# Optimization experiments

Hardware: AMD Instinct MI355X
Metric: run time of the kernel (lower is better)

The kernel has to match this reference:

```python
import jax, jax.numpy as jnp
import numpy as np

BETA = 0.25  # commitment_beta


def _mlp(x, Ws, bs):
    # hidden layers with ReLU, final linear layer without activation
    h = x
    for W, b in zip(Ws[:-1], bs[:-1]):
        h = jax.nn.relu(h @ W + b)
    return h @ Ws[-1] + bs[-1]


def _vq(r, cb):
    # r: [B, D], cb: [K, D]
    # squared L2 distances via expansion: ||r||^2 - 2 r.cb^T + ||cb||^2
    d = (jnp.sum(r * r, axis=1, keepdims=True)
         - 2.0 * (r @ cb.T)
         + jnp.sum(cb * cb, axis=1))  # [B, K]
    idx = jnp.argmin(d, axis=1)  # [B]
    e = cb[idx]  # [B, D]
    sg = jax.lax.stop_gradient
    # per-sample codebook + commitment loss
    loss = (jnp.mean((sg(r) - e) ** 2, axis=1)
            + BETA * jnp.mean((r - sg(e)) ** 2, axis=1))  # [B]
    # straight-through estimator
    z_q = r + sg(e - r)
    return z_q, loss, idx


def setup_inputs() -> dict:
    key = jax.random.key(0)
    ks = jax.random.split(key, 16)
    B, D_IN, H1, H2, D_LAT, K = 16384, 2048, 1024, 512, 256, 1024

    def lin(k, fan_in, fan_out):
        s = 1.0 / np.sqrt(fan_in)
        return jax.random.uniform(k, (fan_in, fan_out), jnp.float32, -s, s)

    return {
        "x": jax.random.normal(ks[0], (B, D_IN), jnp.float32),
        "enc_W1": lin(ks[1], D_IN, H1), "enc_b1": jnp.zeros((H1,), jnp.float32),
        "enc_W2": lin(ks[2], H1, H2), "enc_b2": jnp.zeros((H2,), jnp.float32),
        "enc_W3": lin(ks[3], H2, D_LAT), "enc_b3": jnp.zeros((D_LAT,), jnp.float32),
        "ln_g": jnp.ones((D_LAT,), jnp.float32),
        "ln_b": jnp.zeros((D_LAT,), jnp.float32),
        "cb0": jax.random.normal(ks[4], (K, D_LAT), jnp.float32) * 0.02,
        "cb1": jax.random.normal(ks[5], (K, D_LAT), jnp.float32) * 0.02,
        "cb2": jax.random.normal(ks[6], (K, D_LAT), jnp.float32) * 0.02,
        "dec_W1": lin(ks[7], D_LAT, H2), "dec_b1": jnp.zeros((H2,), jnp.float32),
        "dec_W2": lin(ks[8], H2, H1), "dec_b2": jnp.zeros((H1,), jnp.float32),
        "dec_W3": lin(ks[9], H1, D_IN), "dec_b3": jnp.zeros((D_IN,), jnp.float32),
    }


def reference(x, enc_W1, enc_b1, enc_W2, enc_b2, enc_W3, enc_b3,
              ln_g, ln_b, cb0, cb1, cb2,
              dec_W1, dec_b1, dec_W2, dec_b2, dec_W3, dec_b3):
    z = _mlp(x, [enc_W1, enc_W2, enc_W3], [enc_b1, enc_b2, enc_b3])
    # LayerNorm over latent dim
    mu = jnp.mean(z, axis=-1, keepdims=True)
    var = jnp.var(z, axis=-1, keepdims=True)
    z = (z - mu) * jax.lax.rsqrt(var + 1e-5) * ln_g + ln_b

    sg = jax.lax.stop_gradient
    residual = z
    z_q_total = jnp.zeros_like(z)
    losses, indices = [], []
    for cb in (cb0, cb1, cb2):
        z_q, vloss, idx = _vq(residual, cb)
        residual = residual - sg(z_q)
        z_q_total = z_q_total + z_q
        losses.append(vloss)
        indices.append(idx)

    x_hat = _mlp(z_q_total, [dec_W1, dec_W2, dec_W3], [dec_b1, dec_b2, dec_b3])
    recon_loss = jnp.mean((x_hat - x) ** 2, axis=1)  # [B]
    loss = jnp.sum(jnp.stack(losses, axis=1), axis=1) + recon_loss  # [B]
    idx_out = jnp.stack(indices, axis=1)  # [B, 3]
    return x_hat, loss, idx_out
```

## Files before the change

kernel.cpp:

```cpp
#include <hip/hip_runtime.h>
#include <stdint.h>

typedef __bf16 bf16x8 __attribute__((ext_vector_type(8)));
typedef _Float16 f16x8 __attribute__((ext_vector_type(8)));
typedef float f32x4 __attribute__((ext_vector_type(4)));

#define BETA 0.25f

__device__ __forceinline__ unsigned short f2bf(float f) {
    __bf16 h = (__bf16)f;
    return __builtin_bit_cast(unsigned short, h);
}

__device__ __forceinline__ unsigned short f2h(float f) {
    _Float16 h = (_Float16)f;
    return __builtin_bit_cast(unsigned short, h);
}

__device__ __forceinline__ void split8(const float* a, uint4& vh, uint4& vl) {
    unsigned h[8], l[8];
#pragma unroll
    for (int j = 0; j < 8; ++j) {
        _Float16 hi = (_Float16)a[j];
        float hf = (float)hi;
        _Float16 lo = (_Float16)((a[j] - hf) * 2048.0f);
        h[j] = (unsigned)__builtin_bit_cast(unsigned short, hi);
        l[j] = (unsigned)__builtin_bit_cast(unsigned short, lo);
    }
    vh.x = h[0] | (h[1] << 16); vh.y = h[2] | (h[3] << 16);
    vh.z = h[4] | (h[5] << 16); vh.w = h[6] | (h[7] << 16);
    vl.x = l[0] | (l[1] << 16); vl.y = l[2] | (l[3] << 16);
    vl.z = l[4] | (l[5] << 16); vl.w = l[6] | (l[7] << 16);
}

__global__ __launch_bounds__(256) void wsplit_t(
    const float* __restrict__ W, unsigned short* __restrict__ WTh,
    unsigned short* __restrict__ WTl, int K, int N)
{
    __shared__ float tile[32][33];
    const int t = threadIdx.x;
    const int n0 = blockIdx.x * 32, k0 = blockIdx.y * 32;
    const int rr = t >> 3, c4 = (t & 7) * 4;
    float4 w = *(const float4*)(W + (size_t)(k0 + rr) * N + n0 + c4);
    tile[rr][c4 + 0] = w.x; tile[rr][c4 + 1] = w.y;
    tile[rr][c4 + 2] = w.z; tile[rr][c4 + 3] = w.w;
    __syncthreads();
    float v[4] = {tile[c4 + 0][rr], tile[c4 + 1][rr],
                  tile[c4 + 2][rr], tile[c4 + 3][rr]};
    unsigned short hh[4], ll[4];
#pragma unroll
    for (int j = 0; j < 4; ++j) {
        float s = v[j] * 32.0f;
        _Float16 hi = (_Float16)s;
        float hf = (float)hi;
        hh[j] = __builtin_bit_cast(unsigned short, hi);
        ll[j] = f2h((s - hf) * 2048.0f);
    }
    ushort4 oh, ol;
    oh.x = hh[0]; oh.y = hh[1]; oh.z = hh[2]; oh.w = hh[3];
    ol.x = ll[0]; ol.y = ll[1]; ol.z = ll[2]; ol.w = ll[3];
    *(ushort4*)(WTh + (size_t)(n0 + rr) * K + k0 + c4) = oh;
    *(ushort4*)(WTl + (size_t)(n0 + rr) * K + k0 + c4) = ol;
}

template <bool AF32, bool RELU, bool OUTSPLIT>
__global__ __launch_bounds__(256, 2) void gemm_f16x2(
    const float* __restrict__ Af,
    const unsigned short* __restrict__ Ah, const unsigned short* __restrict__ Al,
    const unsigned short* __restrict__ WTh, const unsigned short* __restrict__ WTl,
    const float* __restrict__ bias,
    void* __restrict__ Oh, unsigned short* __restrict__ Ol,
    int M, int N, int K)
{
    __shared__ unsigned short Ash[2][128][36];
    __shared__ unsigned short Asl[2][128][36];
    __shared__ unsigned short Bsh[2][128][36];
    __shared__ unsigned short Bsl[2][128][36];

    const int t = threadIdx.x;
    const int m0 = blockIdx.y * 128, n0 = blockIdx.x * 128;
    const int wave = t >> 6, lane = t & 63;
    const int wm = wave & 1, wn = wave >> 1;
    const int l15 = lane & 15, kq = lane >> 4;

    f32x4 ach[4][4] = {};
    f32x4 acl[4][4] = {};

    const int sr = t >> 1, skc = (t & 1) * 16;

    float af[16];
    uint4 vah, vah2, val, val2;
    uint4 vbh, vbh2, vbl, vbl2;

    auto LOAD = [&](int kb) {
        if (AF32) {
            const float* ap = Af + (size_t)(m0 + sr) * K + kb + skc;
            *(float4*)&af[0]  = *(const float4*)(ap);
            *(float4*)&af[4]  = *(const float4*)(ap + 4);
            *(float4*)&af[8]  = *(const float4*)(ap + 8);
            *(float4*)&af[12] = *(const float4*)(ap + 12);
        } else {
            const unsigned short* aph = Ah + (size_t)(m0 + sr) * K + kb + skc;
            const unsigned short* apl = Al + (size_t)(m0 + sr) * K + kb + skc;
            vah  = *(const uint4*)(aph);
            vah2 = *(const uint4*)(aph + 8);
            val  = *(const uint4*)(apl);
            val2 = *(const uint4*)(apl + 8);
        }
        const unsigned short* bph = WTh + (size_t)(n0 + sr) * K + kb + skc;
        const unsigned short* bpl = WTl + (size_t)(n0 + sr) * K + kb + skc;
        vbh  = *(const uint4*)(bph);
        vbh2 = *(const uint4*)(bph + 8);
        vbl  = *(const uint4*)(bpl);
        vbl2 = *(const uint4*)(bpl + 8);
    };

    auto STORE = [&](int buf) {
        uint4 wah, wah2, wal, wal2;
        if (AF32) {
            split8(&af[0], wah, wal);
            split8(&af[8], wah2, wal2);
        } else {
            wah = vah; wah2 = vah2; wal = val; wal2 = val2;
        }
        *(uint4*)&Ash[buf][sr][skc]     = wah;
        *(uint4*)&Ash[buf][sr][skc + 8] = wah2;
        *(uint4*)&Asl[buf][sr][skc]     = wal;
        *(uint4*)&Asl[buf][sr][skc + 8] = wal2;
        *(uint4*)&Bsh[buf][sr][skc]     = vbh;
        *(uint4*)&Bsh[buf][sr][skc + 8] = vbh2;
        *(uint4*)&Bsl[buf][sr][skc]     = vbl;
        *(uint4*)&Bsl[buf][sr][skc + 8] = vbl2;
    };

    const int nt = K >> 5;
    LOAD(0);
    STORE(0);
    int cur = 0;
    for (int ti = 0; ti < nt; ++ti) {
        __syncthreads();
        if (ti + 1 < nt) LOAD((ti + 1) << 5);

        f16x8 bh[4], bl[4];
#pragma unroll
        for (int bn = 0; bn < 4; ++bn) {
            bh[bn] = *(const f16x8*)&Bsh[cur][wn * 64 + bn * 16 + l15][kq * 8];
            bl[bn] = *(const f16x8*)&Bsl[cur][wn * 64 + bn * 16 + l15][kq * 8];
        }
#pragma unroll
        for (int am = 0; am < 4; ++am) {
            f16x8 ah_ = *(const f16x8*)&Ash[cur][wm * 64 + am * 16 + l15][kq * 8];
            f16x8 al_ = *(const f16x8*)&Asl[cur][wm * 64 + am * 16 + l15][kq * 8];
#pragma unroll
            for (int bn = 0; bn < 4; ++bn) {
                ach[am][bn] = __builtin_amdgcn_mfma_f32_16x16x32_f16(ah_, bh[bn], ach[am][bn], 0, 0, 0);
                acl[am][bn] = __builtin_amdgcn_mfma_f32_16x16x32_f16(ah_, bl[bn], acl[am][bn], 0, 0, 0);
                acl[am][bn] = __builtin_amdgcn_mfma_f32_16x16x32_f16(al_, bh[bn], acl[am][bn], 0, 0, 0);
            }
        }
        if (ti + 1 < nt) STORE(cur ^ 1);
        cur ^= 1;
    }

#pragma unroll
    for (int am = 0; am < 4; ++am)
#pragma unroll
        for (int bn = 0; bn < 4; ++bn)
#pragma unroll
            for (int r = 0; r < 4; ++r) {
                int row = m0 + wm * 64 + am * 16 + kq * 4 + r;
                int col = n0 + wn * 64 + bn * 16 + l15;
                float v = (ach[am][bn][r] + acl[am][bn][r] * (1.0f / 2048.0f))
                          * (1.0f / 32.0f) + bias[col];
                if (RELU) v = fmaxf(v, 0.0f);
                if (OUTSPLIT) {
                    _Float16 hi = (_Float16)v;
                    float hf = (float)hi;
                    ((unsigned short*)Oh)[(size_t)row * N + col] =
                        __builtin_bit_cast(unsigned short, hi);
                    Ol[(size_t)row * N + col] = f2h((v - hf) * 2048.0f);
                } else {
                    ((float*)Oh)[(size_t)row * N + col] = v;
                }
            }
}

template <bool AF32, bool RELU, bool OUTF32>
__global__ __launch_bounds__(256) void gemm_mfma(
    const void* __restrict__ Av, const float* __restrict__ W,
    const float* __restrict__ bias, void* __restrict__ Ov,
    int M, int N, int K)
{
    __shared__ unsigned short As[64][40];
    __shared__ unsigned short Bs[64][40];

    const int t = threadIdx.x;
    const int m0 = blockIdx.y * 64;
    const int n0 = blockIdx.x * 64;
    const int wave = t >> 6, lane = t & 63;
    const int wm = wave & 1, wn = wave >> 1;
    const int l15 = lane & 15, kq = lane >> 4;

    f32x4 acc[2][2] = {};

    const int sm = t >> 2, skc = t & 3;
    const int sk = t & 31, sng = t >> 5;

    for (int kb = 0; kb < K; kb += 32) {
        uint4 va;
        if (AF32) {
            const float* A = (const float*)Av;
            const float4* p = (const float4*)(A + (size_t)(m0 + sm) * K + kb + skc * 8);
            float4 a0 = p[0], a1 = p[1];
            va.x = (unsigned int)f2bf(a0.x) | ((unsigned int)f2bf(a0.y) << 16);
            va.y = (unsigned int)f2bf(a0.z) | ((unsigned int)f2bf(a0.w) << 16);
            va.z = (unsigned int)f2bf(a1.x) | ((unsigned int)f2bf(a1.y) << 16);
            va.w = (unsigned int)f2bf(a1.z) | ((unsigned int)f2bf(a1.w) << 16);
        } else {
            const unsigned short* A = (const unsigned short*)Av;
            va = *(const uint4*)(A + (size_t)(m0 + sm) * K + kb + skc * 8);
        }
        const float4* wp = (const float4*)(W + (size_t)(kb + sk) * N + n0 + sng * 8);
        float4 w0 = wp[0], w1 = wp[1];
        unsigned short e[8] = {f2bf(w0.x), f2bf(w0.y), f2bf(w0.z), f2bf(w0.w),
                               f2bf(w1.x), f2bf(w1.y), f2bf(w1.z), f2bf(w1.w)};

        __syncthreads();
        *(uint4*)&As[sm][skc * 8] = va;
#pragma unroll
        for (int j = 0; j < 8; ++j) Bs[sng * 8 + j][sk] = e[j];
        __syncthreads();

#pragma unroll
        for (int am = 0; am < 2; ++am) {
            bf16x8 af = *(const bf16x8*)&As[wm * 32 + am * 16 + l15][kq * 8];
#pragma unroll
            for (int bn = 0; bn < 2; ++bn) {
                bf16x8 bfr = *(const bf16x8*)&Bs[wn * 32 + bn * 16 + l15][kq * 8];
                acc[am][bn] = __builtin_amdgcn_mfma_f32_16x16x32_bf16(af, bfr, acc[am][bn], 0, 0, 0);
            }
        }
    }

#pragma unroll
    for (int am = 0; am < 2; ++am)
#pragma unroll
        for (int bn = 0; bn < 2; ++bn)
#pragma unroll
            for (int r = 0; r < 4; ++r) {
                int row = m0 + wm * 32 + am * 16 + kq * 4 + r;
                int col = n0 + wn * 32 + bn * 16 + l15;
                float v = acc[am][bn][r] + bias[col];
                if (RELU) v = fmaxf(v, 0.0f);
                if (OUTF32)
                    ((float*)Ov)[(size_t)row * N + col] = v;
                else
                    ((unsigned short*)Ov)[(size_t)row * N + col] = f2bf(v);
            }
}

template <bool RELU, bool OUTF32>
__global__ __launch_bounds__(256) void gemm_bt128(
    const unsigned short* __restrict__ A, const unsigned short* __restrict__ WT,
    const float* __restrict__ bias, void* __restrict__ Ov,
    int M, int N, int K)
{
    __shared__ unsigned short As[2][128][36];
    __shared__ unsigned short Bs[2][128][36];

    const int t = threadIdx.x;
    const int m0 = blockIdx.y * 128, n0 = blockIdx.x * 128;
    const int wave = t >> 6, lane = t & 63;
    const int wm = wave & 1, wn = wave >> 1;
    const int l15 = lane & 15, kq = lane >> 4;

    f32x4 acc[4][4] = {};

    const int sr = t >> 1, skc = (t & 1) * 16;

    uint4 va, va2, vb, vb2;
    auto LOAD = [&](int kb) {
        const unsigned short* ap = A + (size_t)(m0 + sr) * K + kb + skc;
        const unsigned short* bp = WT + (size_t)(n0 + sr) * K + kb + skc;
        va  = *(const uint4*)(ap);
        va2 = *(const uint4*)(ap + 8);
        vb  = *(const uint4*)(bp);
        vb2 = *(const uint4*)(bp + 8);
    };
    auto STORE = [&](int buf) {
        *(uint4*)&As[buf][sr][skc]     = va;
        *(uint4*)&As[buf][sr][skc + 8] = va2;
        *(uint4*)&Bs[buf][sr][skc]     = vb;
        *(uint4*)&Bs[buf][sr][skc + 8] = vb2;
    };

    const int nt = K >> 5;
    LOAD(0);
    STORE(0);
    int cur = 0;
    for (int ti = 0; ti < nt; ++ti) {
        __syncthreads();
        if (ti + 1 < nt) LOAD((ti + 1) << 5);

        bf16x8 bfr[4];
#pragma unroll
        for (int bn = 0; bn < 4; ++bn)
            bfr[bn] = *(const bf16x8*)&Bs[cur][wn * 64 + bn * 16 + l15][kq * 8];
#pragma unroll
        for (int am = 0; am < 4; ++am) {
            bf16x8 af = *(const bf16x8*)&As[cur][wm * 64 + am * 16 + l15][kq * 8];
#pragma unroll
            for (int bn = 0; bn < 4; ++bn)
                acc[am][bn] = __builtin_amdgcn_mfma_f32_16x16x32_bf16(af, bfr[bn], acc[am][bn], 0, 0, 0);
        }
        if (ti + 1 < nt) STORE(cur ^ 1);
        cur ^= 1;
    }

#pragma unroll
    for (int am = 0; am < 4; ++am)
#pragma unroll
        for (int bn = 0; bn < 4; ++bn)
#pragma unroll
            for (int r = 0; r < 4; ++r) {
                int row = m0 + wm * 64 + am * 16 + kq * 4 + r;
                int col = n0 + wn * 64 + bn * 16 + l15;
                float v = acc[am][bn][r] + bias[col];
                if (RELU) v = fmaxf(v, 0.0f);
                if (OUTF32)
                    ((float*)Ov)[(size_t)row * N + col] = v;
                else
                    ((unsigned short*)Ov)[(size_t)row * N + col] = f2bf(v);
            }
}

__global__ __launch_bounds__(256) void wtrans(
    const float* __restrict__ W, unsigned short* __restrict__ WT, int K, int N)
{
    __shared__ unsigned short tile[32][33];
    const int t = threadIdx.x;
    const int n0 = blockIdx.x * 32, k0 = blockIdx.y * 32;
    const int r = t >> 3, c4 = (t & 7) * 4;
    float4 w = *(const float4*)(W + (size_t)(k0 + r) * N + n0 + c4);
    tile[r][c4 + 0] = f2bf(w.x);
    tile[r][c4 + 1] = f2bf(w.y);
    tile[r][c4 + 2] = f2bf(w.z);
    tile[r][c4 + 3] = f2bf(w.w);
    __syncthreads();
    ushort4 o;
    o.x = tile[c4 + 0][r]; o.y = tile[c4 + 1][r];
    o.z = tile[c4 + 2][r]; o.w = tile[c4 + 3][r];
    *(ushort4*)(WT + (size_t)(n0 + r) * K + k0 + c4) = o;
}

__global__ __launch_bounds__(256) void ln_kernel(
    const float* __restrict__ Z, const float* __restrict__ g,
    const float* __restrict__ b, float* __restrict__ R)
{
    int row = blockIdx.x * 4 + (threadIdx.x >> 6);
    int lane = threadIdx.x & 63;
    float4 v = *(const float4*)(Z + (size_t)row * 256 + lane * 4);
    float s = v.x + v.y + v.z + v.w;
#pragma unroll
    for (int o = 32; o; o >>= 1) s += __shfl_xor(s, o);
    float mu = s * (1.0f / 256.0f);
    float4 d = {v.x - mu, v.y - mu, v.z - mu, v.w - mu};
    float q = d.x * d.x + d.y * d.y + d.z * d.z + d.w * d.w;
#pragma unroll
    for (int o = 32; o; o >>= 1) q += __shfl_xor(q, o);
    float var = q * (1.0f / 256.0f);
    float rs = 1.0f / sqrtf(var + 1e-5f);
    int c0 = lane * 4;
    float4 gg = *(const float4*)(g + c0);
    float4 bb = *(const float4*)(b + c0);
    float4 o4;
    o4.x = d.x * rs * gg.x + bb.x;
    o4.y = d.y * rs * gg.y + bb.y;
    o4.z = d.z * rs * gg.z + bb.z;
    o4.w = d.w * rs * gg.w + bb.w;
    *(float4*)(R + (size_t)row * 256 + c0) = o4;
}

__global__ __launch_bounds__(256) void cninit_kernel(
    const float* __restrict__ CB, float* __restrict__ cn,
    unsigned long long* __restrict__ amin)
{
    int g = blockIdx.x * 256 + threadIdx.x;
    amin[g] = 0xFFFFFFFFFFFFFFFFULL;
    if (g < 1024) {
        const float* p = CB + (size_t)g * 256;
        float s = 0.f;
        for (int d = 0; d < 256; ++d) s = fmaf(p[d], p[d], s);
        cn[g] = s;
    }
}

__global__ __launch_bounds__(256) void rn_kernel(
    const float* __restrict__ R, float* __restrict__ rn)
{
    __shared__ float rs[16][260];
    const int t = threadIdx.x, r0 = blockIdx.x * 16;
    {
        int row = t >> 4, j = t & 15;
#pragma unroll
        for (int q = 0; q < 4; ++q) {
            int col = j * 16 + q * 4;
            *(float4*)&rs[row][col] = *(const float4*)(R + (size_t)(r0 + row) * 256 + col);
        }
    }
    __syncthreads();
    if (t < 16) {
        float s = 0.f;
        for (int d = 0; d < 256; ++d) s = fmaf(rs[t][d], rs[t][d], s);
        rn[r0 + t] = s;
    }
}

__global__ __launch_bounds__(256) void vq_dist(
    const float* __restrict__ Rbuf, const float* __restrict__ CB,
    const float* __restrict__ rn, const float* __restrict__ cn,
    unsigned long long* __restrict__ amin)
{
    __shared__ float As[16][132];
    __shared__ float Bs[16][132];
    __shared__ unsigned long long red[128][17];

    const int t = threadIdx.x;
    const int m0 = blockIdx.y * 128, n0 = blockIdx.x * 128;
    const int tx = t & 15, ty = t >> 4;
    float c[8][8] = {};

    const int sr = t >> 1, skc = (t & 1) * 8;

    for (int kb = 0; kb < 256; kb += 16) {
        const float* ap = Rbuf + (size_t)(m0 + sr) * 256 + kb + skc;
        float4 a0 = *(const float4*)(ap);
        float4 a1 = *(const float4*)(ap + 4);
        const float* bp = CB + (size_t)(n0 + sr) * 256 + kb + skc;
        float4 b0 = *(const float4*)(bp);
        float4 b1 = *(const float4*)(bp + 4);

        __syncthreads();
        As[skc + 0][sr] = a0.x; As[skc + 1][sr] = a0.y;
        As[skc + 2][sr] = a0.z; As[skc + 3][sr] = a0.w;
        As[skc + 4][sr] = a1.x; As[skc + 5][sr] = a1.y;
        As[skc + 6][sr] = a1.z; As[skc + 7][sr] = a1.w;
        Bs[skc + 0][sr] = b0.x; Bs[skc + 1][sr] = b0.y;
        Bs[skc + 2][sr] = b0.z; Bs[skc + 3][sr] = b0.w;
        Bs[skc + 4][sr] = b1.x; Bs[skc + 5][sr] = b1.y;
        Bs[skc + 6][sr] = b1.z; Bs[skc + 7][sr] = b1.w;
        __syncthreads();

#pragma unroll
        for (int k = 0; k < 16; ++k) {
            float a[8], b[8];
            *(float4*)&a[0] = *(const float4*)&As[k][ty * 8];
            *(float4*)&a[4] = *(const float4*)&As[k][ty * 8 + 4];
            *(float4*)&b[0] = *(const float4*)&Bs[k][tx * 4];
            *(float4*)&b[4] = *(const float4*)&Bs[k][64 + tx * 4];
#pragma unroll
            for (int i = 0; i < 8; ++i)
#pragma unroll
                for (int j = 0; j < 8; ++j)
                    c[i][j] = fmaf(a[i], b[j], c[i][j]);
        }
    }

    float rnv[8], cnv[8];
    *(float4*)&rnv[0] = *(const float4*)(rn + m0 + ty * 8);
    *(float4*)&rnv[4] = *(const float4*)(rn + m0 + ty * 8 + 4);
    *(float4*)&cnv[0] = *(const float4*)(cn + n0 + tx * 4);
    *(float4*)&cnv[4] = *(const float4*)(cn + n0 + 64 + tx * 4);

#pragma unroll
    for (int i = 0; i < 8; ++i) {
        unsigned long long best = 0xFFFFFFFFFFFFFFFFULL;
#pragma unroll
        for (int j = 0; j < 8; ++j) {
            float dist = (rnv[i] - 2.0f * c[i][j]) + cnv[j];
            int col = n0 + (j < 4 ? tx * 4 + j : 64 + tx * 4 + (j - 4));
            unsigned long long p =
                ((unsigned long long)__builtin_bit_cast(unsigned int, dist) << 32) |
                (unsigned int)col;
            if (p < best) best = p;
        }
        red[ty * 8 + i][tx] = best;
    }
    __syncthreads();
    if (t < 128) {
        unsigned long long b = red[t][0];
#pragma unroll
        for (int j = 1; j < 16; ++j) {
            unsigned long long v = red[t][j];
            if (v < b) b = v;
        }
        atomicMin(amin + m0 + t, b);
    }
}

__global__ __launch_bounds__(256) void vq_update(
    float* __restrict__ Rbuf, float* __restrict__ ZQ, float* __restrict__ lossf,
    const float* __restrict__ CB, const unsigned long long* __restrict__ amin,
    float* __restrict__ idx_out, int stage)
{
    __shared__ float lred[16][17];
    const int t = threadIdx.x, r0 = blockIdx.x * 16;
    const int row = r0 + (t >> 4), c16 = (t & 15) * 16;
    unsigned int idx = (unsigned int)(amin[row] & 0xffffffffu);
    const float* e = CB + (size_t)idx * 256 + c16;
    float* rp = Rbuf + (size_t)row * 256 + c16;
    float* zp = ZQ + (size_t)row * 256 + c16;
    float part = 0.f;
#pragma unroll
    for (int q = 0; q < 4; ++q) {
        float4 ev = *(const float4*)(e + q * 4);
        float4 rv = *(const float4*)(rp + q * 4);
        float4 dv = {rv.x - ev.x, rv.y - ev.y, rv.z - ev.z, rv.w - ev.w};
        *(float4*)(rp + q * 4) = dv;
        if (stage == 0) {
            *(float4*)(zp + q * 4) = ev;
        } else {
            float4 zv = *(const float4*)(zp + q * 4);
            zv.x += ev.x; zv.y += ev.y; zv.z += ev.z; zv.w += ev.w;
            *(float4*)(zp + q * 4) = zv;
        }
        part = fmaf(dv.x, dv.x, part);
        part = fmaf(dv.y, dv.y, part);
        part = fmaf(dv.z, dv.z, part);
        part = fmaf(dv.w, dv.w, part);
    }
    lred[t >> 4][t & 15] = part;
    __syncthreads();
    if (t < 16) {
        float s = 0.f;
        for (int j = 0; j < 16; ++j) s += lred[t][j];
        float m = s * (1.0f / 256.0f);
        float l = m + BETA * m;
        int gr = r0 + t;
        if (stage == 0) lossf[gr] = l;
        else            lossf[gr] += l;
        idx_out[(size_t)gr * 3 + stage] =
            (float)(unsigned int)(amin[gr] & 0xffffffffu);
    }
}

__global__ __launch_bounds__(256) void recon_kernel(
    const float* __restrict__ XH, const float* __restrict__ X,
    const float* __restrict__ LOSS_IN, float* __restrict__ LOSS_OUT)
{
    __shared__ float wsum[4];
    int row = blockIdx.x, t = threadIdx.x;
    float4 h0 = *(const float4*)(XH + (size_t)row * 2048 + t * 8);
    float4 h1 = *(const float4*)(XH + (size_t)row * 2048 + t * 8 + 4);
    float4 x0 = *(const float4*)(X + (size_t)row * 2048 + t * 8);
    float4 x1 = *(const float4*)(X + (size_t)row * 2048 + t * 8 + 4);
    float h[8] = {h0.x, h0.y, h0.z, h0.w, h1.x, h1.y, h1.z, h1.w};
    float xv[8] = {x0.x, x0.y, x0.z, x0.w, x1.x, x1.y, x1.z, x1.w};
    float s = 0.f;
#pragma unroll
    for (int j = 0; j < 8; ++j) {
        float d = h[j] - xv[j];
        s = fmaf(d, d, s);
    }
#pragma unroll
    for (int o = 32; o; o >>= 1) s += __shfl_xor(s, o);
    if ((t & 63) == 0) wsum[t >> 6] = s;
    __syncthreads();
    if (t == 0) {
        float tot = wsum[0] + wsum[1] + wsum[2] + wsum[3];
        LOSS_OUT[row] = LOSS_IN[row] + tot * (1.0f / 2048.0f);
    }
}

extern "C" void kernel_launch(void* const* d_in, const int* in_sizes, int n_in,
                              void* d_out, int out_size, void* d_ws, size_t ws_size,
                              hipStream_t stream)
{
    const float* x      = (const float*)d_in[0];
    const float* enc_W1 = (const float*)d_in[1];
    const float* enc_b1 = (const float*)d_in[2];
    const float* enc_W2 = (const float*)d_in[3];
    const float* enc_b2 = (const float*)d_in[4];
    const float* enc_W3 = (const float*)d_in[5];
    const float* enc_b3 = (const float*)d_in[6];
    const float* ln_g   = (const float*)d_in[7];
    const float* ln_b   = (const float*)d_in[8];
    const float* cb0    = (const float*)d_in[9];
    const float* cb1    = (const float*)d_in[10];
    const float* cb2    = (const float*)d_in[11];
    const float* dec_W1 = (const float*)d_in[12];
    const float* dec_b1 = (const float*)d_in[13];
    const float* dec_W2 = (const float*)d_in[14];
    const float* dec_b2 = (const float*)d_in[15];
    const float* dec_W3 = (const float*)d_in[16];
    const float* dec_b3 = (const float*)d_in[17];

    const int B = 16384, D_IN = 2048, H1 = 1024, H2 = 512, D_LAT = 256;

    char* ws = (char*)d_ws;
    unsigned short* h1h = (unsigned short*)(ws);
    unsigned short* h1l = (unsigned short*)(ws + (32u << 20));
    unsigned short* h2h = (unsigned short*)(ws + (64u << 20));
    unsigned short* h2l = (unsigned short*)(ws + (80u << 20));
    float* z     = (float*)(ws + (96u << 20));
    float* r     = (float*)(ws + (112u << 20));
    float* zq    = (float*)(ws + (96u << 20));
    unsigned short* w1th = (unsigned short*)(ws + (96u << 20));
    unsigned short* w1tl = (unsigned short*)(ws + (100u << 20));
    unsigned short* w2th = (unsigned short*)(ws + (104u << 20));
    unsigned short* w2tl = (unsigned short*)(ws + (105u << 20));
    unsigned short* w3th = (unsigned short*)(ws + (112u << 20));
    unsigned short* w3tl = (unsigned short*)(ws + (113u << 20));
    unsigned short* d1  = (unsigned short*)(ws);
    unsigned short* d2  = (unsigned short*)(ws + (16u << 20));
    unsigned short* wt3 = (unsigned short*)(ws + (48u << 20));
    unsigned short* wt2 = (unsigned short*)(ws + (52u << 20));
    float* lossf = (float*)(ws + (64u << 20));
    float* cn    = (float*)(ws + (65u << 20));
    unsigned long long* amin = (unsigned long long*)(ws + (66u << 20));
    float* rnb   = (float*)(ws + (67u << 20));

    float* xhat     = (float*)d_out;
    float* loss_out = xhat + (size_t)B * D_IN;
    float* idx_out  = loss_out + B;

    wsplit_t<<<dim3(H1 / 32, D_IN / 32), 256, 0, stream>>>(enc_W1, w1th, w1tl, D_IN, H1);
    wsplit_t<<<dim3(H2 / 32, H1 / 32), 256, 0, stream>>>(enc_W2, w2th, w2tl, H1, H2);
    wsplit_t<<<dim3(D_LAT / 32, H2 / 32), 256, 0, stream>>>(enc_W3, w3th, w3tl, H2, D_LAT);

    gemm_f16x2<true, true, true><<<dim3(H1 / 128, B / 128), 256, 0, stream>>>(
        x, nullptr, nullptr, w1th, w1tl, enc_b1, h1h, h1l, B, H1, D_IN);
    gemm_f16x2<false, true, true><<<dim3(H2 / 128, B / 128), 256, 0, stream>>>(
        nullptr, h1h, h1l, w2th, w2tl, enc_b2, h2h, h2l, B, H2, H1);
    wtrans<<<dim3(H1 / 32, H2 / 32), 256, 0, stream>>>(dec_W2, wt2, H2, H1);
    wtrans<<<dim3(D_IN / 32, H1 / 32), 256, 0, stream>>>(dec_W3, wt3, H1, D_IN);
    gemm_f16x2<false, false, false><<<dim3(D_LAT / 128, B / 128), 256, 0, stream>>>(
        nullptr, h2h, h2l, w3th, w3tl, enc_b3, z, nullptr, B, D_LAT, H2);
    ln_kernel<<<B / 4, 256, 0, stream>>>(z, ln_g, ln_b, r);

    const float* cbs[3] = {cb0, cb1, cb2};
    for (int s = 0; s < 3; ++s) {
        cninit_kernel<<<64, 256, 0, stream>>>(cbs[s], cn, amin);
        rn_kernel<<<B / 16, 256, 0, stream>>>(r, rnb);
        vq_dist<<<dim3(1024 / 128, B / 128), 256, 0, stream>>>(r, cbs[s], rnb, cn, amin);
        vq_update<<<B / 16, 256, 0, stream>>>(r, zq, lossf, cbs[s], amin, idx_out, s);
    }

    gemm_mfma<true, true, false><<<dim3(H2 / 64, B / 64), 256, 0, stream>>>(
        zq, dec_W1, dec_b1, d1, B, H2, D_LAT);
    gemm_bt128<true, false><<<dim3(H1 / 128, B / 128), 256, 0, stream>>>(
        d1, wt2, dec_b2, d2, B, H1, H2);
    gemm_bt128<false, true><<<dim3(D_IN / 128, B / 128), 256, 0, stream>>>(
        d2, wt3, dec_b3, xhat, B, D_IN, H1);
    recon_kernel<<<B, 256, 0, stream>>>(xhat, x, lossf, loss_out);
}
```

Before: 1.182 ms.

## Double-buffer VQ distance tiles, batch codebook norms, use bf16 zq decoder GEMM

The VQ distance kernel now double-buffers its shared-memory tiles, so the next K-slice is loaded from global memory while the current one is computed. Its reduction buffer is aliased onto the same shared memory. The three per-stage codebook-norm and argmin-init launches become one batched launch. The last VQ stage writes the summed zq directly as bf16, which lets the first decoder layer use the pretransposed 128-tile bf16 GEMM in place of the 64-tile fp32-input MFMA kernel. This adds a weight transpose launch and extra workspace buffers.

Result: slower. 1.330 ms (+12.5%).

```diff
diff --git a/kernel.cpp b/kernel.cpp
--- a/kernel.cpp
+++ b/kernel.cpp
@@ -185,80 +185,6 @@
             }
 }
 
-template <bool AF32, bool RELU, bool OUTF32>
-__global__ __launch_bounds__(256) void gemm_mfma(
-    const void* __restrict__ Av, const float* __restrict__ W,
-    const float* __restrict__ bias, void* __restrict__ Ov,
-    int M, int N, int K)
-{
-    __shared__ unsigned short As[64][40];
-    __shared__ unsigned short Bs[64][40];
-
-    const int t = threadIdx.x;
-    const int m0 = blockIdx.y * 64;
-    const int n0 = blockIdx.x * 64;
-    const int wave = t >> 6, lane = t & 63;
-    const int wm = wave & 1, wn = wave >> 1;
-    const int l15 = lane & 15, kq = lane >> 4;
-
-    f32x4 acc[2][2] = {};
-
-    const int sm = t >> 2, skc = t & 3;
-    const int sk = t & 31, sng = t >> 5;
-
-    for (int kb = 0; kb < K; kb += 32) {
-        uint4 va;
-        if (AF32) {
-            const float* A = (const float*)Av;
-            const float4* p = (const float4*)(A + (size_t)(m0 + sm) * K + kb + skc * 8);
-            float4 a0 = p[0], a1 = p[1];
-            va.x = (unsigned int)f2bf(a0.x) | ((unsigned int)f2bf(a0.y) << 16);
-            va.y = (unsigned int)f2bf(a0.z) | ((unsigned int)f2bf(a0.w) << 16);
-            va.z = (unsigned int)f2bf(a1.x) | ((unsigned int)f2bf(a1.y) << 16);
-            va.w = (unsigned int)f2bf(a1.z) | ((unsigned int)f2bf(a1.w) << 16);
-        } else {
-            const unsigned short* A = (const unsigned short*)Av;
-            va = *(const uint4*)(A + (size_t)(m0 + sm) * K + kb + skc * 8);
-        }
-        const float4* wp = (const float4*)(W + (size_t)(kb + sk) * N + n0 + sng * 8);
-        float4 w0 = wp[0], w1 = wp[1];
-        unsigned short e[8] = {f2bf(w0.x), f2bf(w0.y), f2bf(w0.z), f2bf(w0.w),
-                               f2bf(w1.x), f2bf(w1.y), f2bf(w1.z), f2bf(w1.w)};
-
-        __syncthreads();
-        *(uint4*)&As[sm][skc * 8] = va;
-#pragma unroll
-        for (int j = 0; j < 8; ++j) Bs[sng * 8 + j][sk] = e[j];
-        __syncthreads();
-
-#pragma unroll
-        for (int am = 0; am < 2; ++am) {
-            bf16x8 af = *(const bf16x8*)&As[wm * 32 + am * 16 + l15][kq * 8];
-#pragma unroll
-            for (int bn = 0; bn < 2; ++bn) {
-                bf16x8 bfr = *(const bf16x8*)&Bs[wn * 32 + bn * 16 + l15][kq * 8];
-                acc[am][bn] = __builtin_amdgcn_mfma_f32_16x16x32_bf16(af, bfr, acc[am][bn], 0, 0, 0);
-            }
-        }
-    }
-
-#pragma unroll
-    for (int am = 0; am < 2; ++am)
-#pragma unroll
-        for (int bn = 0; bn < 2; ++bn)
-#pragma unroll
-            for (int r = 0; r < 4; ++r) {
-                int row = m0 + wm * 32 + am * 16 + kq * 4 + r;
-                int col = n0 + wn * 32 + bn * 16 + l15;
-                float v = acc[am][bn][r] + bias[col];
-                if (RELU) v = fmaxf(v, 0.0f);
-                if (OUTF32)
-                    ((float*)Ov)[(size_t)row * N + col] = v;
-                else
-                    ((unsigned short*)Ov)[(size_t)row * N + col] = f2bf(v);
-            }
-}
-
 template <bool RELU, bool OUTF32>
 __global__ __launch_bounds__(256) void gemm_bt128(
     const unsigned short* __restrict__ A, const unsigned short* __restrict__ WT,
@@ -381,17 +307,21 @@
     *(float4*)(R + (size_t)row * 256 + c0) = o4;
 }
 
-__global__ __launch_bounds__(256) void cninit_kernel(
-    const float* __restrict__ CB, float* __restrict__ cn,
+__global__ __launch_bounds__(256) void cninit3(
+    const float* __restrict__ CB0, const float* __restrict__ CB1,
+    const float* __restrict__ CB2, float* __restrict__ cn,
     unsigned long long* __restrict__ amin)
 {
-    int g = blockIdx.x * 256 + threadIdx.x;
-    amin[g] = 0xFFFFFFFFFFFFFFFFULL;
+    int b = blockIdx.x;
+    int s = b >> 6, lb = b & 63;
+    int g = lb * 256 + threadIdx.x;
+    amin[(size_t)s * 16384 + g] = 0xFFFFFFFFFFFFFFFFULL;
     if (g < 1024) {
+        const float* CB = (s == 0) ? CB0 : (s == 1) ? CB1 : CB2;
         const float* p = CB + (size_t)g * 256;
-        float s = 0.f;
-        for (int d = 0; d < 256; ++d) s = fmaf(p[d], p[d], s);
-        cn[g] = s;
+        float sum = 0.f;
+        for (int d = 0; d < 256; ++d) sum = fmaf(p[d], p[d], sum);
+        cn[s * 1024 + g] = sum;
     }
 }
 
@@ -421,9 +351,10 @@
     const float* __restrict__ rn, const float* __restrict__ cn,
     unsigned long long* __restrict__ amin)
 {
-    __shared__ float As[16][132];
-    __shared__ float Bs[16][132];
-    __shared__ unsigned long long red[128][17];
+    __shared__ char smem[33792];
+    float (*As)[16][132] = (float (*)[16][132])smem;
+    float (*Bs)[16][132] = (float (*)[16][132])(smem + 16896);
+    unsigned long long (*red)[17] = (unsigned long long (*)[17])smem;
 
     const int t = threadIdx.x;
     const int m0 = blockIdx.y * 128, n0 = blockIdx.x * 128;
@@ -432,38 +363,48 @@
 
     const int sr = t >> 1, skc = (t & 1) * 8;
 
-    for (int kb = 0; kb < 256; kb += 16) {
+    float4 a0, a1, b0, b1;
+    auto LOAD = [&](int kb) {
         const float* ap = Rbuf + (size_t)(m0 + sr) * 256 + kb + skc;
-        float4 a0 = *(const float4*)(ap);
-        float4 a1 = *(const float4*)(ap + 4);
+        a0 = *(const float4*)(ap);
+        a1 = *(const float4*)(ap + 4);
         const float* bp = CB + (size_t)(n0 + sr) * 256 + kb + skc;
-        float4 b0 = *(const float4*)(bp);
-        float4 b1 = *(const float4*)(bp + 4);
-
+        b0 = *(const float4*)(bp);
+        b1 = *(const float4*)(bp + 4);
+    };
+    auto STORE = [&](int buf) {
+        As[buf][skc + 0][sr] = a0.x; As[buf][skc + 1][sr] = a0.y;
+        As[buf][skc + 2][sr] = a0.z; As[buf][skc + 3][sr] = a0.w;
+        As[buf][skc + 4][sr] = a1.x; As[buf][skc + 5][sr] = a1.y;
+        As[buf][skc + 6][sr] = a1.z; As[buf][skc + 7][sr] = a1.w;
+        Bs[buf][skc + 0][sr] = b0.x; Bs[buf][skc + 1][sr] = b0.y;
+        Bs[buf][skc + 2][sr] = b0.z; Bs[buf][skc + 3][sr] = b0.w;
+        Bs[buf][skc + 4][sr] = b1.x; Bs[buf][skc + 5][sr] = b1.y;
+        Bs[buf][skc + 6][sr] = b1.z; Bs[buf][skc + 7][sr] = b1.w;
+    };
+
+    LOAD(0);
+    STORE(0);
+    int cur = 0;
+    for (int ti = 0; ti < 16; ++ti) {
         __syncthreads();
-        As[skc + 0][sr] = a0.x; As[skc + 1][sr] = a0.y;
-        As[skc + 2][sr] = a0.z; As[skc + 3][sr] = a0.w;
-        As[skc + 4][sr] = a1.x; As[skc + 5][sr] = a1.y;
-        As[skc + 6][sr] = a1.z; As[skc + 7][sr] = a1.w;
-        Bs[skc + 0][sr] = b0.x; Bs[skc + 1][sr] = b0.y;
-        Bs[skc + 2][sr] = b0.z; Bs[skc + 3][sr] = b0.w;
-        Bs[skc + 4][sr] = b1.x; Bs[skc + 5][sr] = b1.y;
-        Bs[skc + 6][sr] = b1.z; Bs[skc + 7][sr] = b1.w;
-        __syncthreads();
+        if (ti + 1 < 16) LOAD((ti + 1) * 16);
 
 #pragma unroll
         for (int k = 0; k < 16; ++k) {
             float a[8], b[8];
-            *(float4*)&a[0] = *(const float4*)&As[k][ty * 8];
-            *(float4*)&a[4] = *(const float4*)&As[k][ty * 8 + 4];
-            *(float4*)&b[0] = *(const float4*)&Bs[k][tx * 4];
-            *(float4*)&b[4] = *(const float4*)&Bs[k][64 + tx * 4];
+            *(float4*)&a[0] = *(const float4*)&As[cur][k][ty * 8];
+            *(float4*)&a[4] = *(const float4*)&As[cur][k][ty * 8 + 4];
+            *(float4*)&b[0] = *(const float4*)&Bs[cur][k][tx * 4];
+            *(float4*)&b[4] = *(const float4*)&Bs[cur][k][64 + tx * 4];
 #pragma unroll
             for (int i = 0; i < 8; ++i)
 #pragma unroll
                 for (int j = 0; j < 8; ++j)
                     c[i][j] = fmaf(a[i], b[j], c[i][j]);
         }
+        if (ti + 1 < 16) STORE(cur ^ 1);
+        cur ^= 1;
     }
 
     float rnv[8], cnv[8];
@@ -471,6 +412,8 @@
     *(float4*)&rnv[4] = *(const float4*)(rn + m0 + ty * 8 + 4);
     *(float4*)&cnv[0] = *(const float4*)(cn + n0 + tx * 4);
     *(float4*)&cnv[4] = *(const float4*)(cn + n0 + 64 + tx * 4);
+
+    __syncthreads();
 
 #pragma unroll
     for (int i = 0; i < 8; ++i) {
@@ -501,7 +444,7 @@
 __global__ __launch_bounds__(256) void vq_update(
     float* __restrict__ Rbuf, float* __restrict__ ZQ, float* __restrict__ lossf,
     const float* __restrict__ CB, const unsigned long long* __restrict__ amin,
-    float* __restrict__ idx_out, int stage)
+    float* __restrict__ idx_out, unsigned short* __restrict__ ZQB, int stage)
 {
     __shared__ float lred[16][17];
     const int t = threadIdx.x, r0 = blockIdx.x * 16;
@@ -519,10 +462,17 @@
         *(float4*)(rp + q * 4) = dv;
         if (stage == 0) {
             *(float4*)(zp + q * 4) = ev;
+        } else if (stage == 1) {
+            float4 zv = *(const float4*)(zp + q * 4);
+            zv.x += ev.x; zv.y += ev.y; zv.z += ev.z; zv.w += ev.w;
+            *(float4*)(zp + q * 4) = zv;
         } else {
             float4 zv = *(const float4*)(zp + q * 4);
             zv.x += ev.x; zv.y += ev.y; zv.z += ev.z; zv.w += ev.w;
-            *(float4*)(zp + q * 4) = zv;
+            ushort4 zb;
+            zb.x = f2bf(zv.x); zb.y = f2bf(zv.y);
+            zb.z = f2bf(zv.z); zb.w = f2bf(zv.w);
+            *(ushort4*)(ZQB + (size_t)row * 256 + c16 + q * 4) = zb;
         }
         part = fmaf(dv.x, dv.x, part);
         part = fmaf(dv.y, dv.y, part);
@@ -616,9 +566,11 @@
     unsigned short* wt3 = (unsigned short*)(ws + (48u << 20));
     unsigned short* wt2 = (unsigned short*)(ws + (52u << 20));
     float* lossf = (float*)(ws + (64u << 20));
-    float* cn    = (float*)(ws + (65u << 20));
-    unsigned long long* amin = (unsigned long long*)(ws + (66u << 20));
+    float* cn3   = (float*)(ws + (65u << 20));
+    unsigned long long* amin3 = (unsigned long long*)(ws + (66u << 20));
     float* rnb   = (float*)(ws + (67u << 20));
+    unsigned short* zqb = (unsigned short*)(ws + (68u << 20));
+    unsigned short* wt1 = (unsigned short*)(ws + (76u << 20));
 
     float* xhat     = (float*)d_out;
     float* loss_out = xhat + (size_t)B * D_IN;
@@ -638,16 +590,20 @@
         nullptr, h2h, h2l, w3th, w3tl, enc_b3, z, nullptr, B, D_LAT, H2);
     ln_kernel<<<B / 4, 256, 0, stream>>>(z, ln_g, ln_b, r);
 
+    cninit3<<<192, 256, 0, stream>>>(cb0, cb1, cb2, cn3, amin3);
+    wtrans<<<dim3(H2 / 32, D_LAT / 32), 256, 0, stream>>>(dec_W1, wt1, D_LAT, H2);
+
     const float* cbs[3] = {cb0, cb1, cb2};
     for (int s = 0; s < 3; ++s) {
-        cninit_kernel<<<64, 256, 0, stream>>>(cbs[s], cn, amin);
         rn_kernel<<<B / 16, 256, 0, stream>>>(r, rnb);
-        vq_dist<<<dim3(1024 / 128, B / 128), 256, 0, stream>>>(r, cbs[s], rnb, cn, amin);
-        vq_update<<<B / 16, 256, 0, stream>>>(r, zq, lossf, cbs[s], amin, idx_out, s);
-    }
-
-    gemm_mfma<true, true, false><<<dim3(H2 / 64, B / 64), 256, 0, stream>>>(
-        zq, dec_W1, dec_b1, d1, B, H2, D_LAT);
+        vq_dist<<<dim3(1024 / 128, B / 128), 256, 0, stream>>>(
+            r, cbs[s], rnb, cn3 + s * 1024, amin3 + (size_t)s * 16384);
+        vq_update<<<B / 16, 256, 0, stream>>>(
+            r, zq, lossf, cbs[s], amin3 + (size_t)s * 16384, idx_out, zqb, s);
+    }
+
+    gemm_bt128<true, false><<<dim3(H2 / 128, B / 128), 256, 0, stream>>>(
+        zqb, wt1, dec_b1, d1, B, H2, D_LAT);
     gemm_bt128<true, false><<<dim3(H1 / 128, B / 128), 256, 0, stream>>>(
         d1, wt2, dec_b2, d2, B, H1, H2);
     gemm_bt128<false, true><<<dim3(D_IN / 128, B / 128), 256, 0, stream>>>(
```
